# Performance work log

Hardware: AMD Instinct MI355X
Metric: run time of the kernel (lower is better)

The kernel has to match this reference:

```python
import jax, jax.numpy as jnp
import numpy as np

B = 64
FEATS = [96, 64, 64, 64]   # per-level input features
NCNT = [1, 8, 64, 512]     # per-level node counts
NODES = 512                # nodes at current depth (tree[-1])
DEG = 8                    # branching degree at this depth
IN_F = 64                  # features[depth]
OUT_F = 64                 # features[depth+1]
SUP = 640                  # in_f * 10 support hidden


def setup_inputs() -> dict:
    key = jax.random.key(0)
    ks = jax.random.split(key, 12)
    inp = {}
    for i in range(4):
        inp[f"x{i}"] = jax.random.normal(ks[i], (B, NCNT[i], FEATS[i]), jnp.float32)
        inp[f"W{i}"] = jax.random.normal(ks[4 + i], (FEATS[i], OUT_F), jnp.float32) / np.sqrt(FEATS[i]).astype(np.float32)
    inp["branch"] = jax.random.normal(ks[8], (NODES, IN_F, IN_F * DEG), jnp.float32) / np.float32(8.0)
    inp["Ws1"] = jax.random.normal(ks[9], (IN_F, SUP), jnp.float32) / np.float32(8.0)
    inp["Ws2"] = jax.random.normal(ks[10], (SUP, OUT_F), jnp.float32) / np.sqrt(SUP).astype(np.float32)
    bound = np.float32(1.0 / np.sqrt(OUT_F))
    inp["bias"] = jax.random.uniform(ks[11], (1, DEG, OUT_F), jnp.float32, -bound, bound)
    return inp


def _lrelu(v):
    return jnp.where(v > 0, v, 0.2 * v)


def reference(x0, x1, x2, x3, W0, W1, W2, W3, branch, Ws1, Ws2, bias):
    xs = [x0, x1, x2, x3]
    Ws = [W0, W1, W2, W3]
    # multi-depth linear sum: project each ancestor level, replicate each
    # node's vector contiguously down to `NODES` rows (torch repeat+view)
    y = jnp.zeros((B, NODES, OUT_F), jnp.float32)
    for x, W in zip(xs, Ws):
        t = x @ W                                   # (B, n_i, OUT_F)
        y = y + jnp.repeat(t, NODES // t.shape[1], axis=1)
    # branching: per-node weight slice (GEMV per node, shared over batch)
    xb = _lrelu(jnp.einsum('bnf,nfg->bng', x3, branch))  # (B, NODES, IN_F*DEG)
    xb = xb.reshape(B, NODES * DEG, IN_F)
    xb = (xb @ Ws1) @ Ws2                           # support MLP -> (B, NODES*DEG, OUT_F)
    y = xb + jnp.repeat(y, DEG, axis=1)             # y repeat(1,1,deg).view
    y = _lrelu(y + jnp.tile(bias, (1, NODES, 1)))   # bias.repeat(1, nodes, 1)
    return y
```

## Files before the change

kernel.cpp:

```cpp
#include <hip/hip_runtime.h>


typedef float f32x4 __attribute__((ext_vector_type(4)));
typedef __bf16 bf16x8 __attribute__((ext_vector_type(8)));

__device__ __forceinline__ unsigned short f2bf(float f) {
    union { float f; unsigned int u; } x; x.f = f;
    unsigned int r = x.u + 0x7FFFu + ((x.u >> 16) & 1u);
    return (unsigned short)(r >> 16);
}

__global__ __launch_bounds__(256) void tree_prep(
    const float* __restrict__ x0, const float* __restrict__ W0,
    const float* __restrict__ x1, const float* __restrict__ W1,
    const float* __restrict__ x2, const float* __restrict__ W2,
    const float* __restrict__ x3, const float* __restrict__ W3,
    const float* __restrict__ Ws1, const float* __restrict__ Ws2,
    float* __restrict__ ylg, unsigned short* __restrict__ xbf,
    unsigned short* __restrict__ wsF, unsigned short* __restrict__ w3f)
{
    const int t = threadIdx.x;
    const int blk = blockIdx.x;
    if (blk < 1024) {
        const int b = blk >> 4;
        const int g = ((blk & 15) << 2) + (t >> 6);
        const int f = t & 63;
        const float* xp = x0 + b * 96;
        float a0 = 0.f, a1 = 0.f;
        #pragma unroll 8
        for (int k = 0; k < 96; k += 2) {
            a0 += xp[k]     * W0[k * 64 + f];
            a1 += xp[k + 1] * W0[(k + 1) * 64 + f];
        }
        const float* x1p = x1 + b * 512 + (g >> 3) * 64;
        #pragma unroll 8
        for (int k = 0; k < 64; k += 2) {
            a0 += x1p[k]     * W1[k * 64 + f];
            a1 += x1p[k + 1] * W1[(k + 1) * 64 + f];
        }
        const float* x2p = x2 + b * 4096 + g * 64;
        #pragma unroll 8
        for (int k = 0; k < 64; k += 2) {
            a0 += x2p[k]     * W2[k * 64 + f];
            a1 += x2p[k + 1] * W2[(k + 1) * 64 + f];
        }
        const int mt = b >> 4, l4 = (b >> 2) & 3, r = b & 3;
        const int ft = f >> 4, l15 = f & 15;
        ylg[(size_t)((g * 4 + mt) * 4 + ft) * 256 + (l4 * 16 + l15) * 4 + r] = a0 + a1;
    } else if (blk < 3072) {
        const int bb = blk - 1024;
        const int b = bb >> 5, ngrp = bb & 31;
        const int n = ngrp * 16 + (t >> 4), k0 = 4 * (t & 15);
        float4 v = *(const float4*)(x3 + (size_t)b * 32768 + (size_t)n * 64 + k0);
        const int mt = b >> 4, l15b = b & 15, ks = k0 >> 5, l4k = (k0 >> 3) & 3, j = k0 & 7;
        union { unsigned short h[4]; uint2 u; } p;
        p.h[0] = f2bf(v.x); p.h[1] = f2bf(v.y); p.h[2] = f2bf(v.z); p.h[3] = f2bf(v.w);
        *(uint2*)&xbf[(size_t)n * 4096 + ((mt * 2 + ks) * 64 + l4k * 16 + l15b) * 8 + j] = p.u;
    } else if (blk < 3136) {
        __shared__ float red[4][64];
        const int c = blk - 3072;
        const int f = t & 63, q = t >> 6;
        const float* w1p = Ws1 + (size_t)c * 640 + q * 160;
        const float* w2p = Ws2 + (size_t)(q * 160) * 64 + f;
        float a0 = 0.f, a1 = 0.f;
        #pragma unroll 8
        for (int s = 0; s < 160; s += 2) {
            a0 += w1p[s]     * w2p[(size_t)s * 64];
            a1 += w1p[s + 1] * w2p[(size_t)(s + 1) * 64];
        }
        red[q][f] = a0 + a1;
        __syncthreads();
        if (q == 0) {
            const float v = red[0][f] + red[1][f] + red[2][f] + red[3][f];
            const int ks = c >> 5, l4c = (c >> 3) & 3, j = c & 7;
            wsF[((f >> 4) * 2 + ks) * 512 + (l4c * 16 + (f & 15)) * 8 + j] = f2bf(v);
        }
    } else {
        const int l = t & 63;
        #pragma unroll
        for (int it = 0; it < 2; ++it) {
            const int fh = it * 4 + (t >> 6);
            const int ft = fh >> 1, ks = fh & 1;
            const int f = ft * 16 + (l & 15);
            const int kb = ks * 32 + (l >> 4) * 8;
            union { unsigned short h[8]; uint4 u; } p;
            #pragma unroll
            for (int j = 0; j < 8; ++j) p.h[j] = f2bf(W3[(kb + j) * 64 + f]);
            *(uint4*)&w3f[((size_t)fh * 64 + l) * 8] = p.u;
        }
    }
}

__global__ __launch_bounds__(64, 3) void tree_main(
    const float* __restrict__ branch, const float* __restrict__ bias,
    const float* __restrict__ ylg, const unsigned short* __restrict__ xbf,
    const unsigned short* __restrict__ wsF, const unsigned short* __restrict__ w3f,
    float* __restrict__ out)
{
    __shared__ unsigned short Bt[16 * 72];
    __shared__ unsigned short Ts[64 * 72];
    const int l = threadIdx.x;
    const int l15 = l & 15, l4 = l >> 4;
    const int n = blockIdx.x >> 3, d = blockIdx.x & 7;
    const int g = n >> 3;
    const int rk = l & 15, cq = l >> 4;

    const float* brp = branch + (size_t)n * 32768 + d * 64 + 4 * cq;

    float4 bl[4];
    #pragma unroll
    for (int i = 0; i < 4; ++i)
        bl[i] = *(const float4*)(brp + (size_t)(4 * rk + i) * 512);

    bf16x8 af[4][2];
    #pragma unroll
    for (int mt = 0; mt < 4; ++mt)
        #pragma unroll
        for (int ks = 0; ks < 2; ++ks)
            af[mt][ks] = *(const bf16x8*)(xbf + (size_t)n * 4096 +
                                          ((mt * 2 + ks) * 64 + l) * 8);

    #pragma unroll
    for (int ct = 0; ct < 4; ++ct) {
        #pragma unroll
        for (int ci = 0; ci < 4; ++ci) {
            union { unsigned short h[4]; uint2 u; } q;
            #pragma unroll
            for (int i = 0; i < 4; ++i) q.h[i] = f2bf(((const float*)&bl[i])[ci]);
            *(uint2*)&Bt[(4 * cq + ci) * 72 + 4 * rk] = q.u;
        }
        if (ct < 3) {
            #pragma unroll
            for (int i = 0; i < 4; ++i)
                bl[i] = *(const float4*)(brp + (size_t)(4 * rk + i) * 512 + 16 * (ct + 1));
        }
        bf16x8 bt0 = *(const bf16x8*)&Bt[l15 * 72 + 8 * l4];
        bf16x8 bt1 = *(const bf16x8*)&Bt[l15 * 72 + 32 + 8 * l4];
        #pragma unroll
        for (int mt = 0; mt < 4; ++mt) {
            f32x4 s = {0.f, 0.f, 0.f, 0.f};
            s = __builtin_amdgcn_mfma_f32_16x16x32_bf16(af[mt][0], bt0, s, 0, 0, 0);
            s = __builtin_amdgcn_mfma_f32_16x16x32_bf16(af[mt][1], bt1, s, 0, 0, 0);
            #pragma unroll
            for (int r = 0; r < 4; ++r) {
                float v = s[r];
                v = fmaxf(v, 0.2f * v);
                Ts[(16 * mt + 4 * l4 + r) * 72 + 16 * ct + l15] = f2bf(v);
            }
        }
    }

    bf16x8 w3[4][2], wf[4][2];
    #pragma unroll
    for (int ft = 0; ft < 4; ++ft)
        #pragma unroll
        for (int ks = 0; ks < 2; ++ks) {
            w3[ft][ks] = *(const bf16x8*)(w3f + (size_t)((ft * 2 + ks) * 64 + l) * 8);
            wf[ft][ks] = *(const bf16x8*)(wsF + (size_t)((ft * 2 + ks) * 64 + l) * 8);
        }
    float bv[4];
    #pragma unroll
    for (int ft = 0; ft < 4; ++ft) bv[ft] = bias[d * 64 + 16 * ft + l15];

    float* outp = out + (size_t)blockIdx.x * 64;
    #pragma unroll
    for (int mt = 0; mt < 4; ++mt) {
        f32x4 y[4];
        #pragma unroll
        for (int ft = 0; ft < 4; ++ft)
            y[ft] = *(const f32x4*)(ylg + (size_t)((g * 4 + mt) * 4 + ft) * 256 + l * 4);
        bf16x8 at0 = *(const bf16x8*)&Ts[(16 * mt + l15) * 72 + 8 * l4];
        bf16x8 at1 = *(const bf16x8*)&Ts[(16 * mt + l15) * 72 + 32 + 8 * l4];
        #pragma unroll
        for (int ft = 0; ft < 4; ++ft) {
            y[ft] = __builtin_amdgcn_mfma_f32_16x16x32_bf16(af[mt][0], w3[ft][0], y[ft], 0, 0, 0);
            y[ft] = __builtin_amdgcn_mfma_f32_16x16x32_bf16(af[mt][1], w3[ft][1], y[ft], 0, 0, 0);
            y[ft] = __builtin_amdgcn_mfma_f32_16x16x32_bf16(at0, wf[ft][0], y[ft], 0, 0, 0);
            y[ft] = __builtin_amdgcn_mfma_f32_16x16x32_bf16(at1, wf[ft][1], y[ft], 0, 0, 0);
        }
        #pragma unroll
        for (int ft = 0; ft < 4; ++ft)
            #pragma unroll
            for (int r = 0; r < 4; ++r) {
                float val = y[ft][r] + bv[ft];
                val = fmaxf(val, 0.2f * val);
                outp[(size_t)(16 * mt + 4 * l4 + r) * 262144 + 16 * ft + l15] = val;
            }
    }
}

extern "C" void kernel_launch(void* const* d_in, const int* in_sizes, int n_in,
                              void* d_out, int out_size, void* d_ws, size_t ws_size,
                              hipStream_t stream) {
    (void)in_sizes; (void)n_in; (void)out_size; (void)ws_size;
    const float* x0     = (const float*)d_in[0];
    const float* W0     = (const float*)d_in[1];
    const float* x1     = (const float*)d_in[2];
    const float* W1     = (const float*)d_in[3];
    const float* x2     = (const float*)d_in[4];
    const float* W2     = (const float*)d_in[5];
    const float* x3     = (const float*)d_in[6];
    const float* W3     = (const float*)d_in[7];
    const float* branch = (const float*)d_in[8];
    const float* Ws1    = (const float*)d_in[9];
    const float* Ws2    = (const float*)d_in[10];
    const float* bias   = (const float*)d_in[11];

    float* ylg          = (float*)d_ws;
    unsigned short* xbf = (unsigned short*)((char*)d_ws + 1048576);
    unsigned short* wsF = (unsigned short*)((char*)d_ws + 5242880);
    unsigned short* w3f = (unsigned short*)((char*)d_ws + 5251072);
    float* out = (float*)d_out;

    tree_prep<<<3137, 256, 0, stream>>>(x0, W0, x1, W1, x2, W2, x3, W3, Ws1, Ws2,
                                        ylg, xbf, wsF, w3f);
    tree_main<<<4096, 64, 0, stream>>>(branch, bias, ylg, xbf, wsF, w3f, out);
}
```

Baseline: 54.04 us.

## Load branch slices directly as MFMA operands and pack four waves per block

The branch GEMM is restructured to read the fp32 branch weights straight into MFMA A-operand layout, converting them to bf16 in registers. This removes the LDS transpose staging buffer Bt and its per-chunk loop, and computes the transposed product (branch^T times x), so the LReLU result is written to LDS with packed 8-byte stores. The kernel now runs four independent waves per 256-thread block (1024 blocks instead of 4096). In exchange, branch loads become scalar strided per-lane reads rather than float4s, and register pressure rises from holding all raw values and 16 accumulators at once.

```diff
diff --git a/kernel.cpp b/kernel.cpp
--- a/kernel.cpp
+++ b/kernel.cpp
@@ -9,6 +9,8 @@
     unsigned int r = x.u + 0x7FFFu + ((x.u >> 16) & 1u);
     return (unsigned short)(r >> 16);
 }
+
+#define LDP 72
 
 __global__ __launch_bounds__(256) void tree_prep(
     const float* __restrict__ x0, const float* __restrict__ W0,
@@ -91,64 +93,74 @@
     }
 }
 
-__global__ __launch_bounds__(64, 3) void tree_main(
+__global__ __launch_bounds__(256, 4) void tree_main(
     const float* __restrict__ branch, const float* __restrict__ bias,
     const float* __restrict__ ylg, const unsigned short* __restrict__ xbf,
     const unsigned short* __restrict__ wsF, const unsigned short* __restrict__ w3f,
     float* __restrict__ out)
 {
-    __shared__ unsigned short Bt[16 * 72];
-    __shared__ unsigned short Ts[64 * 72];
-    const int l = threadIdx.x;
+    __shared__ unsigned short Ts[4][64 * LDP];
+    const int t = threadIdx.x;
+    const int w = t >> 6, l = t & 63;
     const int l15 = l & 15, l4 = l >> 4;
-    const int n = blockIdx.x >> 3, d = blockIdx.x & 7;
+    const int id = blockIdx.x * 4 + w;
+    const int n = id >> 3, d = id & 7;
     const int g = n >> 3;
-    const int rk = l & 15, cq = l >> 4;
-
-    const float* brp = branch + (size_t)n * 32768 + d * 64 + 4 * cq;
-
-    float4 bl[4];
-    #pragma unroll
-    for (int i = 0; i < 4; ++i)
-        bl[i] = *(const float4*)(brp + (size_t)(4 * rk + i) * 512);
-
-    bf16x8 af[4][2];
-    #pragma unroll
-    for (int mt = 0; mt < 4; ++mt)
+    unsigned short* ts = Ts[w];
+
+    const float* brp = branch + (size_t)n * 32768 + d * 64;
+    float raw[4][2][8];
+    #pragma unroll
+    for (int cP = 0; cP < 4; ++cP)
         #pragma unroll
         for (int ks = 0; ks < 2; ++ks)
-            af[mt][ks] = *(const bf16x8*)(xbf + (size_t)n * 4096 +
-                                          ((mt * 2 + ks) * 64 + l) * 8);
-
-    #pragma unroll
-    for (int ct = 0; ct < 4; ++ct) {
-        #pragma unroll
-        for (int ci = 0; ci < 4; ++ci) {
+            #pragma unroll
+            for (int j = 0; j < 8; ++j)
+                raw[cP][ks][j] = brp[(size_t)(32 * ks + 8 * l4 + j) * 512 + 16 * cP + l15];
+
+    bf16x8 bx[4][2];
+    #pragma unroll
+    for (int bt = 0; bt < 4; ++bt)
+        #pragma unroll
+        for (int ks = 0; ks < 2; ++ks)
+            bx[bt][ks] = *(const bf16x8*)(xbf + (size_t)n * 4096 +
+                                          ((bt * 2 + ks) * 64 + l) * 8);
+
+    bf16x8 pf[4][2];
+    #pragma unroll
+    for (int cP = 0; cP < 4; ++cP)
+        #pragma unroll
+        for (int ks = 0; ks < 2; ++ks) {
+            union { unsigned short h[8]; bf16x8 bv; } p;
+            #pragma unroll
+            for (int j = 0; j < 8; ++j) p.h[j] = f2bf(raw[cP][ks][j]);
+            pf[cP][ks] = p.bv;
+        }
+
+    f32x4 st[4][4];
+    #pragma unroll
+    for (int cP = 0; cP < 4; ++cP)
+        #pragma unroll
+        for (int bt = 0; bt < 4; ++bt) {
+            f32x4 acc = {0.f, 0.f, 0.f, 0.f};
+            acc = __builtin_amdgcn_mfma_f32_16x16x32_bf16(pf[cP][0], bx[bt][0], acc, 0, 0, 0);
+            acc = __builtin_amdgcn_mfma_f32_16x16x32_bf16(pf[cP][1], bx[bt][1], acc, 0, 0, 0);
+            st[cP][bt] = acc;
+        }
+
+    #pragma unroll
+    for (int bt = 0; bt < 4; ++bt)
+        #pragma unroll
+        for (int cP = 0; cP < 4; ++cP) {
             union { unsigned short h[4]; uint2 u; } q;
             #pragma unroll
-            for (int i = 0; i < 4; ++i) q.h[i] = f2bf(((const float*)&bl[i])[ci]);
-            *(uint2*)&Bt[(4 * cq + ci) * 72 + 4 * rk] = q.u;
-        }
-        if (ct < 3) {
-            #pragma unroll
-            for (int i = 0; i < 4; ++i)
-                bl[i] = *(const float4*)(brp + (size_t)(4 * rk + i) * 512 + 16 * (ct + 1));
-        }
-        bf16x8 bt0 = *(const bf16x8*)&Bt[l15 * 72 + 8 * l4];
-        bf16x8 bt1 = *(const bf16x8*)&Bt[l15 * 72 + 32 + 8 * l4];
-        #pragma unroll
-        for (int mt = 0; mt < 4; ++mt) {
-            f32x4 s = {0.f, 0.f, 0.f, 0.f};
-            s = __builtin_amdgcn_mfma_f32_16x16x32_bf16(af[mt][0], bt0, s, 0, 0, 0);
-            s = __builtin_amdgcn_mfma_f32_16x16x32_bf16(af[mt][1], bt1, s, 0, 0, 0);
-            #pragma unroll
             for (int r = 0; r < 4; ++r) {
-                float v = s[r];
+                float v = st[cP][bt][r];
                 v = fmaxf(v, 0.2f * v);
-                Ts[(16 * mt + 4 * l4 + r) * 72 + 16 * ct + l15] = f2bf(v);
+                q.h[r] = f2bf(v);
             }
-        }
-    }
+            *(uint2*)&ts[(16 * bt + l15) * LDP + 16 * cP + 4 * l4] = q.u;
+        }
 
     bf16x8 w3[4][2], wf[4][2];
     #pragma unroll
@@ -162,21 +174,21 @@
     #pragma unroll
     for (int ft = 0; ft < 4; ++ft) bv[ft] = bias[d * 64 + 16 * ft + l15];
 
-    float* outp = out + (size_t)blockIdx.x * 64;
-    #pragma unroll
-    for (int mt = 0; mt < 4; ++mt) {
+    float* outp = out + (size_t)(n * 8 + d) * 64;
+    #pragma unroll
+    for (int bt = 0; bt < 4; ++bt) {
         f32x4 y[4];
         #pragma unroll
         for (int ft = 0; ft < 4; ++ft)
-            y[ft] = *(const f32x4*)(ylg + (size_t)((g * 4 + mt) * 4 + ft) * 256 + l * 4);
-        bf16x8 at0 = *(const bf16x8*)&Ts[(16 * mt + l15) * 72 + 8 * l4];
-        bf16x8 at1 = *(const bf16x8*)&Ts[(16 * mt + l15) * 72 + 32 + 8 * l4];
+            y[ft] = *(const f32x4*)(ylg + (size_t)((g * 4 + bt) * 4 + ft) * 256 + l * 4);
+        bf16x8 a20 = *(const bf16x8*)&ts[(16 * bt + l15) * LDP + 8 * l4];
+        bf16x8 a21 = *(const bf16x8*)&ts[(16 * bt + l15) * LDP + 32 + 8 * l4];
         #pragma unroll
         for (int ft = 0; ft < 4; ++ft) {
-            y[ft] = __builtin_amdgcn_mfma_f32_16x16x32_bf16(af[mt][0], w3[ft][0], y[ft], 0, 0, 0);
-            y[ft] = __builtin_amdgcn_mfma_f32_16x16x32_bf16(af[mt][1], w3[ft][1], y[ft], 0, 0, 0);
-            y[ft] = __builtin_amdgcn_mfma_f32_16x16x32_bf16(at0, wf[ft][0], y[ft], 0, 0, 0);
-            y[ft] = __builtin_amdgcn_mfma_f32_16x16x32_bf16(at1, wf[ft][1], y[ft], 0, 0, 0);
+            y[ft] = __builtin_amdgcn_mfma_f32_16x16x32_bf16(bx[bt][0], w3[ft][0], y[ft], 0, 0, 0);
+            y[ft] = __builtin_amdgcn_mfma_f32_16x16x32_bf16(bx[bt][1], w3[ft][1], y[ft], 0, 0, 0);
+            y[ft] = __builtin_amdgcn_mfma_f32_16x16x32_bf16(a20, wf[ft][0], y[ft], 0, 0, 0);
+            y[ft] = __builtin_amdgcn_mfma_f32_16x16x32_bf16(a21, wf[ft][1], y[ft], 0, 0, 0);
         }
         #pragma unroll
         for (int ft = 0; ft < 4; ++ft)
@@ -184,7 +196,7 @@
             for (int r = 0; r < 4; ++r) {
                 float val = y[ft][r] + bv[ft];
                 val = fmaxf(val, 0.2f * val);
-                outp[(size_t)(16 * mt + 4 * l4 + r) * 262144 + 16 * ft + l15] = val;
+                outp[(size_t)(16 * bt + 4 * l4 + r) * 262144 + 16 * ft + l15] = val;
             }
     }
 }
@@ -214,5 +226,5 @@
 
     tree_prep<<<3137, 256, 0, stream>>>(x0, W0, x1, W1, x2, W2, x3, W3, Ws1, Ws2,
                                         ylg, xbf, wsF, w3f);
-    tree_main<<<4096, 64, 0, stream>>>(branch, bias, ylg, xbf, wsF, w3f, out);
-}
+    tree_main<<<1024, 256, 0, stream>>>(branch, bias, ylg, xbf, wsF, w3f, out);
+}
```

New measurement: 60.27 us. 11.5% more time.
